# Performance work log

Hardware: AMD Instinct MI355X
Metric: run time of the kernel (lower is better)

Reference implementation:

```python
import jax, jax.numpy as jnp
import numpy as np
from jax import lax

NL = 2        # num mamba layers
D_MODEL = 200
D_STATE = 16
D_CONV = 4
DI = 400      # expand * d_model
DT_RANK = 13  # ceil(d_model / 16)
B = 256
L = 256
EPS = 1e-12


def _ln(x, w, b):
    mu = jnp.mean(x, axis=-1, keepdims=True)
    var = jnp.mean((x - mu) ** 2, axis=-1, keepdims=True)
    return (x - mu) / jnp.sqrt(var + EPS) * w + b


def _mamba(x, in_proj_w, conv_w, conv_b, x_proj_w, dt_proj_w, dt_proj_b, A_log, D, out_proj_w):
    b, l, _ = x.shape
    xz = jnp.einsum('bld,ed->ble', x, in_proj_w)  # [b,l,2*DI]
    xc, z = jnp.split(xz, 2, axis=-1)
    # causal depthwise conv over time (pad d_conv-1 on the left == pytorch pad+slice)
    xt = xc.transpose(0, 2, 1)  # [b,DI,l]
    xt = lax.conv_general_dilated(xt, conv_w[:, None, :], (1,), [(D_CONV - 1, 0)],
                                  dimension_numbers=('NCH', 'OIH', 'NCH'),
                                  feature_group_count=DI)
    xc = jax.nn.silu(xt + conv_b[None, :, None]).transpose(0, 2, 1)  # [b,l,DI]
    x_dbl = jnp.einsum('bld,ed->ble', xc, x_proj_w)  # [b,l,DT_RANK+2*N]
    dt = x_dbl[..., :DT_RANK]
    Bm = x_dbl[..., DT_RANK:DT_RANK + D_STATE]
    Cm = x_dbl[..., DT_RANK + D_STATE:]
    delta = jax.nn.softplus(jnp.einsum('blr,dr->bld', dt, dt_proj_w) + dt_proj_b)  # [b,l,DI]
    A = -jnp.exp(A_log)  # [DI,N]

    def step(h, inp):
        d_t, u_t, B_t, C_t = inp  # [b,DI],[b,DI],[b,N],[b,N]
        dA = jnp.exp(d_t[..., None] * A)  # [b,DI,N]
        h = dA * h + (d_t * u_t)[..., None] * B_t[:, None, :]
        y = jnp.einsum('bdn,bn->bd', h, C_t)
        return h, y

    h0 = jnp.zeros((b, DI, D_STATE), dtype=x.dtype)
    xs = (delta.transpose(1, 0, 2), xc.transpose(1, 0, 2),
          Bm.transpose(1, 0, 2), Cm.transpose(1, 0, 2))
    _, ys = lax.scan(step, h0, xs)
    y = ys.transpose(1, 0, 2) + xc * D  # [b,l,DI]
    y = y * jax.nn.silu(z)
    return jnp.einsum('bld,ed->ble', y, out_proj_w)


def _forward(item_emb, in_proj_w, conv_w, conv_b, x_proj_w, dt_proj_w, dt_proj_b,
             A_log, D, out_proj_w, ln1_w, ln1_b, ffn_w1, ffn_b1, ffn_w2, ffn_b2,
             ffn_ln_w, ffn_ln_b):
    h = item_emb
    for i in range(NL):
        m = _mamba(h, in_proj_w[i], conv_w[i], conv_b[i], x_proj_w[i],
                   dt_proj_w[i], dt_proj_b[i], A_log[i], D[i], out_proj_w[i])
        h = _ln(m + h, ln1_w[i], ln1_b[i])  # num_layers > 1 -> residual branch
        f = jnp.einsum('bld,ed->ble', h, ffn_w1[i]) + ffn_b1[i]
        f = jax.nn.gelu(f, approximate=False)  # torch nn.GELU default = exact
        f = jnp.einsum('ble,de->bld', f, ffn_w2[i]) + ffn_b2[i]
        h = _ln(f + h, ffn_ln_w[i], ffn_ln_b[i])
    c = h[:, -1:, :]
    x_n = h[:, :-1, :]
    return c, x_n


def setup_inputs() -> dict:
    key = jax.random.key(0)
    ks = jax.random.split(key, 10)
    s = 0.02
    f32 = jnp.float32
    A_log = jnp.broadcast_to(jnp.log(jnp.arange(1, D_STATE + 1, dtype=f32)),
                             (NL, DI, D_STATE))
    return {
        'item_emb': jax.random.normal(ks[0], (B, L, D_MODEL), f32),
        'item_seq_len': jax.random.randint(ks[1], (B,), 1, L, jnp.int32),
        'in_proj_w': s * jax.random.normal(ks[2], (NL, 2 * DI, D_MODEL), f32),
        'conv_w': s * jax.random.normal(ks[3], (NL, DI, D_CONV), f32),
        'conv_b': jnp.zeros((NL, DI), f32),
        'x_proj_w': s * jax.random.normal(ks[4], (NL, DT_RANK + 2 * D_STATE, DI), f32),
        'dt_proj_w': s * jax.random.normal(ks[5], (NL, DI, DT_RANK), f32),
        'dt_proj_b': s * jax.random.normal(ks[6], (NL, DI), f32),
        'A_log': A_log,
        'D': jnp.ones((NL, DI), f32),
        'out_proj_w': s * jax.random.normal(ks[7], (NL, D_MODEL, DI), f32),
        'ln1_w': jnp.ones((NL, D_MODEL), f32),
        'ln1_b': jnp.zeros((NL, D_MODEL), f32),
        'ffn_w1': s * jax.random.normal(ks[8], (NL, 4 * D_MODEL, D_MODEL), f32),
        'ffn_b1': jnp.zeros((NL, 4 * D_MODEL), f32),
        'ffn_w2': s * jax.random.normal(ks[9], (NL, D_MODEL, 4 * D_MODEL), f32),
        'ffn_b2': jnp.zeros((NL, D_MODEL), f32),
        'ffn_ln_w': jnp.ones((NL, D_MODEL), f32),
        'ffn_ln_b': jnp.zeros((NL, D_MODEL), f32),
    }


def reference(item_emb, item_seq_len, in_proj_w, conv_w, conv_b, x_proj_w,
              dt_proj_w, dt_proj_b, A_log, D, out_proj_w, ln1_w, ln1_b,
              ffn_w1, ffn_b1, ffn_w2, ffn_b2, ffn_ln_w, ffn_ln_b):
    # item_seq_len is accepted but unused by Mamba4Rec.forward
    return _forward(item_emb, in_proj_w, conv_w, conv_b, x_proj_w, dt_proj_w,
                    dt_proj_b, A_log, D, out_proj_w, ln1_w, ln1_b, ffn_w1,
                    ffn_b1, ffn_w2, ffn_b2, ffn_ln_w, ffn_ln_b)
```

## Files before the change

kernel.cpp:

```cpp
#include <hip/hip_runtime.h>
#include <hip/hip_bf16.h>

#define DM 200
#define DIE 400
#define LSEQ 256
#define NB 256

typedef __hip_bfloat16 bf16;
typedef const float* fp;
typedef __attribute__((ext_vector_type(8))) short short8;
typedef __attribute__((ext_vector_type(4))) short short4_t;
typedef __attribute__((ext_vector_type(4))) float f32x4;

__device__ __forceinline__ float b2f(bf16 x) { return __bfloat162float(x); }
__device__ __forceinline__ bf16  f2b(float x) { return __float2bfloat16(x); }

__device__ __forceinline__ unsigned short f2bbits(float f) {
    union { float f; unsigned int u; } c; c.f = f;
    unsigned int u = c.u;
    unsigned int r = (u + 0x7fffu + ((u >> 16) & 1u)) >> 16;
    return (unsigned short)r;
}
__device__ __forceinline__ void stf(float* p, float v) { *p = v; }
__device__ __forceinline__ void stf(bf16* p, float v) { *p = f2b(v); }

#define W_XP_OFF 320000
#define W_OP_OFF 356000
#define W_F1_OFF 516000
#define W_F2_OFF 836000
#define W_TOTAL  1156000
#define W_BYTES  2312000

__global__ __launch_bounds__(256) void wcvt_kernel(fp a0, fp a1, fp a2, fp a3, fp a4,
                                                   bf16* __restrict__ dst) {
    int g = blockIdx.x * 256 + threadIdx.x;
    if (g >= W_TOTAL / 4) return;
    int idx = g * 4;
    const float* src;
    int off;
    if (idx < W_XP_OFF)      { src = a0; off = idx; }
    else if (idx < W_OP_OFF) { src = a1; off = idx - W_XP_OFF; }
    else if (idx < W_F1_OFF) { src = a2; off = idx - W_OP_OFF; }
    else if (idx < W_F2_OFF) { src = a3; off = idx - W_F1_OFF; }
    else                     { src = a4; off = idx - W_F2_OFF; }
    float4 v = *(const float4*)(src + off);
    short4_t o;
    o.x = (short)f2bbits(v.x); o.y = (short)f2bbits(v.y);
    o.z = (short)f2bbits(v.z); o.w = (short)f2bbits(v.w);
    *(short4_t*)((short*)dst + idx) = o;
}

__global__ __launch_bounds__(256) void cvt_kernel(const float* __restrict__ src,
                                                  bf16* __restrict__ dst, int n4) {
    int g = blockIdx.x * 256 + threadIdx.x;
    if (g >= n4) return;
    int idx = g * 4;
    float4 v = *(const float4*)(src + idx);
    short4_t o;
    o.x = (short)f2bbits(v.x); o.y = (short)f2bbits(v.y);
    o.z = (short)f2bbits(v.z); o.w = (short)f2bbits(v.w);
    *(short4_t*)((short*)dst + idx) = o;
}

template <typename TC, int EPI>
__global__ __launch_bounds__(256) void gemm_mfma(const bf16* __restrict__ A, int lda,
                                                 const bf16* __restrict__ W,
                                                 const float* __restrict__ bias,
                                                 TC* __restrict__ C, int ldc,
                                                 int N, int K) {
    constexpr int LS = 40;
    __shared__ short As[128 * LS];
    __shared__ short Bs[128 * LS];
    const int m0 = blockIdx.x * 128;
    const int n0 = blockIdx.y * 128;
    const int tid = threadIdx.x;
    const int wave = tid >> 6;
    const int lane = tid & 63;
    const int wm = (wave & 1) * 64;
    const int wn = (wave >> 1) * 64;
    const int fm = lane & 15;
    const int quad = lane >> 4;

    f32x4 acc[4][4] = {};

    const int sr = tid >> 1;
    const int sc = (tid & 1) * 16;

    for (int k0 = 0; k0 < K; k0 += 32) {
        {
            const short* src = (const short*)A + (size_t)(m0 + sr) * lda + k0 + sc;
            short* dst = As + sr * LS + sc;
            if (k0 + sc + 16 <= K) {
                *(short8*)dst = *(const short8*)src;
                *(short8*)(dst + 8) = *(const short8*)(src + 8);
            } else {
#pragma unroll
                for (int j = 0; j < 16; ++j)
                    dst[j] = (k0 + sc + j < K) ? src[j] : (short)0;
            }
        }
        {
            short* dst = Bs + sr * LS + sc;
            if (n0 + sr < N) {
                const short* src = (const short*)W + (size_t)(n0 + sr) * K + k0 + sc;
                if (k0 + sc + 16 <= K) {
                    *(short8*)dst = *(const short8*)src;
                    *(short8*)(dst + 8) = *(const short8*)(src + 8);
                } else {
#pragma unroll
                    for (int j = 0; j < 16; ++j)
                        dst[j] = (k0 + sc + j < K) ? src[j] : (short)0;
                }
            } else {
#pragma unroll
                for (int j = 0; j < 16; ++j) dst[j] = 0;
            }
        }
        __syncthreads();
        short8 af[4], bfr[4];
#pragma unroll
        for (int i = 0; i < 4; ++i)
            af[i] = *(const short8*)(As + (wm + i * 16 + fm) * LS + quad * 8);
#pragma unroll
        for (int j = 0; j < 4; ++j)
            bfr[j] = *(const short8*)(Bs + (wn + j * 16 + fm) * LS + quad * 8);
#pragma unroll
        for (int i = 0; i < 4; ++i)
#pragma unroll
            for (int j = 0; j < 4; ++j)
                acc[i][j] = __builtin_amdgcn_mfma_f32_16x16x32_bf16(af[i], bfr[j], acc[i][j], 0, 0, 0);
        __syncthreads();
    }

#pragma unroll
    for (int j = 0; j < 4; ++j) {
        int n = n0 + wn + j * 16 + fm;
        if (n >= N) continue;
        float bv = (EPI == 2 || EPI == 3) ? bias[n] : 0.f;
#pragma unroll
        for (int i = 0; i < 4; ++i) {
#pragma unroll
            for (int r = 0; r < 4; ++r) {
                int m = m0 + wm + i * 16 + quad * 4 + r;
                float v = acc[i][j][r];
                if (EPI == 2) {
                    v += bv;
                    v = 0.5f * v * (1.f + erff(v * 0.70710678118654752f));
                } else if (EPI == 3) {
                    v += bv;
                } else if (EPI == 5) {
                    if (n >= 400) v = v * __builtin_amdgcn_rcpf(1.f + __expf(-v));
                }
                stf(&C[(size_t)m * ldc + n], v);
            }
        }
    }
}

__global__ __launch_bounds__(256) void conv_silu_inplace(bf16* __restrict__ xz,
                                                         const float* __restrict__ cw,
                                                         const float* __restrict__ cb,
                                                         int total ) {
    int idx = blockIdx.x * 256 + threadIdx.x;
    if (idx >= total) return;
    int d = idx % DIE;
    int b = idx / DIE;
    float w0 = cw[d * 4 + 0];
    float w1 = cw[d * 4 + 1];
    float w2 = cw[d * 4 + 2];
    float w3 = cw[d * 4 + 3];
    float bias = cb[d];
    float x0 = 0.f, x1 = 0.f, x2 = 0.f;
    bf16* p = xz + (size_t)b * LSEQ * 800 + d;
    for (int t = 0; t < LSEQ; ++t) {
        float x = b2f(*p);
        float s = bias + w0 * x0 + w1 * x1 + w2 * x2 + w3 * x;
        x0 = x1; x1 = x2; x2 = x;
        float sig = __builtin_amdgcn_rcpf(1.f + __expf(-s));
        *p = f2b(s * sig);
        p += 800;
    }
}

template <bool FAST>
__device__ __forceinline__ void scan_body(const float* __restrict__ rp,
                                          bf16* __restrict__ xp,
                                          const float* Wr, const float* A2,
                                          float bdt, float Dv) {
    float h[16];
#pragma unroll
    for (int n = 0; n < 16; ++n) h[n] = 0.f;

    auto precomp = [&](int o45, int ox,
                       float* Bb, float* Cb, float* dA, float& du, float& ut, float& zs) {
        float dtv = bdt;
#pragma unroll
        for (int r = 0; r < 13; ++r) dtv += Wr[r] * rp[o45 + r];
#pragma unroll
        for (int j = 0; j < 16; ++j) { Bb[j] = rp[o45 + 13 + j]; Cb[j] = rp[o45 + 29 + j]; }
        ut = b2f(xp[ox]);
        zs = b2f(xp[ox + 400]);
        float sp = (dtv > 20.f) ? dtv : __logf(1.f + __expf(dtv));
        if (FAST) {
            float r1 = __expf(-sp);
            float r2 = r1 * r1, r3 = r2 * r1, r4 = r2 * r2;
            float r5 = r4 * r1, r6 = r4 * r2, r7 = r4 * r3, r8 = r4 * r4;
            dA[0] = r1;  dA[1] = r2;  dA[2] = r3;  dA[3] = r4;
            dA[4] = r5;  dA[5] = r6;  dA[6] = r7;  dA[7] = r8;
            dA[8] = r8 * r1;  dA[9] = r8 * r2;  dA[10] = r8 * r3;  dA[11] = r8 * r4;
            dA[12] = r8 * r5; dA[13] = r8 * r6; dA[14] = r8 * r7;  dA[15] = r8 * r8;
        } else {
#pragma unroll
            for (int n = 0; n < 16; ++n) dA[n] = __expf(sp * A2[n]);
        }
        du = sp * ut;
    };
    auto compute = [&](const float* Bb, const float* Cb, const float* dA,
                       float du, float ut, float zs, int ox) {
#pragma unroll
        for (int n = 0; n < 16; ++n) h[n] = dA[n] * h[n] + du * Bb[n];
        float y0 = 0.f, y1 = 0.f, y2 = 0.f, y3 = 0.f;
#pragma unroll
        for (int n = 0; n < 4; ++n) {
            y0 += h[n] * Cb[n];
            y1 += h[4 + n] * Cb[4 + n];
            y2 += h[8 + n] * Cb[8 + n];
            y3 += h[12 + n] * Cb[12 + n];
        }
        float yv = (y0 + y1) + (y2 + y3) + ut * Dv;
        xp[ox] = f2b(yv * zs);
    };

    float BA[16], CA[16], dAA[16], BB[16], CB[16], dAB[16];
    float duA, utA, zsA, duB, utB, zsB;

    precomp(0, 0, BA, CA, dAA, duA, utA, zsA);

    for (int t = 0; t < LSEQ; t += 2) {
        precomp(45, 800, BB, CB, dAB, duB, utB, zsB);
        compute(BA, CA, dAA, duA, utA, zsA, 0);
        if (t + 2 < LSEQ)
            precomp(90, 1600, BA, CA, dAA, duA, utA, zsA);
        compute(BB, CB, dAB, duB, utB, zsB, 800);
        rp += 90; xp += 1600;
    }
}

__global__ __launch_bounds__(256) void scan_kernel(const float* __restrict__ xdbl,
                                                   bf16* __restrict__ xz,
                                                   const float* __restrict__ dt_w,
                                                   const float* __restrict__ dt_b,
                                                   const float* __restrict__ A_log,
                                                   const float* __restrict__ Dw) {
    const int b = blockIdx.x >> 1;
    const int half = blockIdx.x & 1;
    const int tid = threadIdx.x;
    if (tid >= 200) return;
    const int d = half * 200 + tid;

    float A2[16], Wr[13];
    bool fast = true;
#pragma unroll
    for (int n = 0; n < 16; ++n) {
        A2[n] = -__expf(A_log[d * 16 + n]);
        fast = fast && (fabsf(A2[n] + (float)(n + 1)) < 1e-3f);
    }
#pragma unroll
    for (int r = 0; r < 13; ++r) Wr[r] = dt_w[d * 13 + r];
    const float bdt = dt_b[d];
    const float Dv = Dw[d];

    const float* __restrict__ rp = xdbl + (size_t)b * LSEQ * 45;
    bf16* __restrict__ xp = xz + (size_t)b * LSEQ * 800 + d;

    if (fast) scan_body<true>(rp, xp, Wr, A2, bdt, Dv);
    else      scan_body<false>(rp, xp, Wr, A2, bdt, Dv);
}

__global__ __launch_bounds__(256) void ln_res_kernel(const float* __restrict__ xa,
                                                     const float* xb,
                                                     const float* __restrict__ w,
                                                     const float* __restrict__ bias,
                                                     float* dst,
                                                     bf16* __restrict__ dstb, int rows,
                                                     float* __restrict__ outp, int b0) {
    int wave = threadIdx.x >> 6;
    int lane = threadIdx.x & 63;
    int row = blockIdx.x * 4 + wave;
    if (row >= rows) return;
    const float* pa = xa + (size_t)row * DM;
    const float* pb = xb + (size_t)row * DM;
    float v[4];
    float sum = 0.f, sq = 0.f;
#pragma unroll
    for (int i = 0; i < 4; ++i) {
        int c = lane + i * 64;
        float t = 0.f;
        if (c < DM) t = pa[c] + pb[c];
        v[i] = t;
        sum += t;
        sq += t * t;
    }
#pragma unroll
    for (int off = 32; off > 0; off >>= 1) {
        sum += __shfl_down(sum, off);
        sq += __shfl_down(sq, off);
    }
    sum = __shfl(sum, 0);
    sq = __shfl(sq, 0);
    float mu = sum * (1.f / DM);
    float var = fmaxf(sq * (1.f / DM) - mu * mu, 0.f);
    float rstd = rsqrtf(var + 1e-12f);
    if (outp) {
        int bb = b0 + row / LSEQ;
        int l = row % LSEQ;
        float* po = (l == LSEQ - 1)
                        ? outp + (size_t)bb * DM
                        : outp + (size_t)NB * DM + (size_t)(bb * (LSEQ - 1) + l) * DM;
#pragma unroll
        for (int i = 0; i < 4; ++i) {
            int c = lane + i * 64;
            if (c < DM) po[c] = (v[i] - mu) * rstd * w[c] + bias[c];
        }
    } else {
        float* pd = dst + (size_t)row * DM;
        bf16* pdb = dstb + (size_t)row * DM;
#pragma unroll
        for (int i = 0; i < 4; ++i) {
            int c = lane + i * 64;
            if (c < DM) {
                float o = (v[i] - mu) * rstd * w[c] + bias[c];
                pd[c] = o;
                pdb[c] = f2b(o);
            }
        }
    }
}

extern "C" void kernel_launch(void* const* d_in, const int* in_sizes, int n_in,
                              void* d_out, int out_size, void* d_ws, size_t ws_size,
                              hipStream_t stream) {
    fp emb       = (fp)d_in[0];
    fp in_proj_w = (fp)d_in[2];
    fp conv_w    = (fp)d_in[3];
    fp conv_b    = (fp)d_in[4];
    fp x_proj_w  = (fp)d_in[5];
    fp dt_proj_w = (fp)d_in[6];
    fp dt_proj_b = (fp)d_in[7];
    fp A_log     = (fp)d_in[8];
    fp Dw        = (fp)d_in[9];
    fp out_proj_w= (fp)d_in[10];
    fp ln1_w     = (fp)d_in[11];
    fp ln1_b     = (fp)d_in[12];
    fp ffn_w1    = (fp)d_in[13];
    fp ffn_b1    = (fp)d_in[14];
    fp ffn_w2    = (fp)d_in[15];
    fp ffn_b2    = (fp)d_in[16];
    fp ffn_ln_w  = (fp)d_in[17];
    fp ffn_ln_b  = (fp)d_in[18];

    const int cands[8] = {256, 128, 64, 32, 16, 8, 4, 2};
    int cb = 2;
    for (int ci = 0; ci < 8; ++ci) {
        size_t rcx = (size_t)cands[ci] * LSEQ;
        if (rcx * 3780 + W_BYTES + 1024 <= ws_size) { cb = cands[ci]; break; }
    }
    const size_t rc = (size_t)cb * LSEQ;

    bf16*  wb   = (bf16*)d_ws;
    bf16*  xz   = (bf16*)((char*)d_ws + W_BYTES);
    bf16*  hb   = xz + rc * 800;
    float* xdbl = (float*)(hb + rc * 200);
    float* m    = xdbl + rc * 45;
    float* h    = m + rc * 200;

    wcvt_kernel<<<(W_TOTAL / 4 + 255) / 256, 256, 0, stream>>>(
        in_proj_w, x_proj_w, out_proj_w, ffn_w1, ffn_w2, wb);

    const int rcDM = (int)rc * DM;
    const int gm = (int)rc / 128;

    for (int b0 = 0; b0 < NB; b0 += cb) {
        const float* emb_chunk = emb + (size_t)b0 * LSEQ * DM;

        cvt_kernel<<<(rcDM / 4 + 255) / 256, 256, 0, stream>>>(emb_chunk, hb, rcDM / 4);

        for (int i = 0; i < 2; ++i) {
            const bf16* wb_in = wb + (size_t)i * 160000;
            const bf16* wb_xp = wb + W_XP_OFF + (size_t)i * 18000;
            const bf16* wb_op = wb + W_OP_OFF + (size_t)i * 80000;
            const bf16* wb_f1 = wb + W_F1_OFF + (size_t)i * 160000;
            const bf16* wb_f2 = wb + W_F2_OFF + (size_t)i * 160000;
            fp cw    = conv_w + (size_t)i * 400 * 4;
            fp cbp   = conv_b + (size_t)i * 400;
            fp w_dt  = dt_proj_w + (size_t)i * 400 * 13;
            fp b_dt  = dt_proj_b + (size_t)i * 400;
            fp Ai    = A_log + (size_t)i * 400 * 16;
            fp Di    = Dw + (size_t)i * 400;
            fp l1w   = ln1_w + (size_t)i * 200;
            fp l1b   = ln1_b + (size_t)i * 200;
            fp f1b   = ffn_b1 + (size_t)i * 800;
            fp f2b_  = ffn_b2 + (size_t)i * 200;
            fp flw   = ffn_ln_w + (size_t)i * 200;
            fp flb   = ffn_ln_b + (size_t)i * 200;

            const float* hin = (i == 0) ? emb_chunk : h;
            const bool last = (i == 1);

            gemm_mfma<bf16, 5><<<dim3(gm, 7), 256, 0, stream>>>(
                hb, 200, wb_in, nullptr, xz, 800, 800, 200);
            conv_silu_inplace<<<(cb * DIE + 255) / 256, 256, 0, stream>>>(xz, cw, cbp, cb * DIE);
            gemm_mfma<float, 0><<<dim3(gm, 1), 256, 0, stream>>>(
                xz, 800, wb_xp, nullptr, xdbl, 45, 45, 400);
            scan_kernel<<<cb * 2, 256, 0, stream>>>(xdbl, xz, w_dt, b_dt, Ai, Di);
            gemm_mfma<float, 0><<<dim3(gm, 2), 256, 0, stream>>>(
                xz, 800, wb_op, nullptr, m, 200, 200, 400);
            ln_res_kernel<<<rc / 4, 256, 0, stream>>>(m, hin, l1w, l1b, h, hb, (int)rc,
                                                      nullptr, 0);
            gemm_mfma<bf16, 2><<<dim3(gm, 7), 256, 0, stream>>>(
                hb, 200, wb_f1, f1b, xz, 800, 800, 200);
            gemm_mfma<float, 3><<<dim3(gm, 2), 256, 0, stream>>>(
                xz, 800, wb_f2, f2b_, m, 200, 200, 800);
            ln_res_kernel<<<rc / 4, 256, 0, stream>>>(m, h, flw, flb, h, hb, (int)rc,
                                                      last ? (float*)d_out : nullptr, b0);
        }
    }
}
```

Measured before the change: 1.311 ms.

## Split scan state dimension across two lanes per channel with shuffle reduction

The selective-scan kernel now assigns two threads per channel, each owning 8 of the 16 state elements, and combines the partial outputs with a lane shuffle. Blocks grow from 256 to 512 threads. This doubles thread-level parallelism and halves per-thread register pressure for the sequential recurrence, aiming to shorten the scan's critical path. The cost is that the dt projection, softplus and loads are computed redundantly in both lanes, and there is an extra shuffle per step.

Result: no change. 1.307 ms (-0.3%).

```diff
diff --git a/kernel.cpp b/kernel.cpp
--- a/kernel.cpp
+++ b/kernel.cpp
@@ -186,10 +186,12 @@
 __device__ __forceinline__ void scan_body(const float* __restrict__ rp,
                                           bf16* __restrict__ xp,
                                           const float* Wr, const float* A2,
-                                          float bdt, float Dv) {
-    float h[16];
-#pragma unroll
-    for (int n = 0; n < 16; ++n) h[n] = 0.f;
+                                          float bdt, float Dv, int sub) {
+    float h[8];
+#pragma unroll
+    for (int n = 0; n < 8; ++n) h[n] = 0.f;
+    const int nbase = 13 + sub * 8;
+    const int cbase = 29 + sub * 8;
 
     auto precomp = [&](int o45, int ox,
                        float* Bb, float* Cb, float* dA, float& du, float& ut, float& zs) {
@@ -197,7 +199,7 @@
 #pragma unroll
         for (int r = 0; r < 13; ++r) dtv += Wr[r] * rp[o45 + r];
 #pragma unroll
-        for (int j = 0; j < 16; ++j) { Bb[j] = rp[o45 + 13 + j]; Cb[j] = rp[o45 + 29 + j]; }
+        for (int j = 0; j < 8; ++j) { Bb[j] = rp[o45 + nbase + j]; Cb[j] = rp[o45 + cbase + j]; }
         ut = b2f(xp[ox]);
         zs = b2f(xp[ox + 400]);
         float sp = (dtv > 20.f) ? dtv : __logf(1.f + __expf(dtv));
@@ -205,33 +207,34 @@
             float r1 = __expf(-sp);
             float r2 = r1 * r1, r3 = r2 * r1, r4 = r2 * r2;
             float r5 = r4 * r1, r6 = r4 * r2, r7 = r4 * r3, r8 = r4 * r4;
-            dA[0] = r1;  dA[1] = r2;  dA[2] = r3;  dA[3] = r4;
-            dA[4] = r5;  dA[5] = r6;  dA[6] = r7;  dA[7] = r8;
-            dA[8] = r8 * r1;  dA[9] = r8 * r2;  dA[10] = r8 * r3;  dA[11] = r8 * r4;
-            dA[12] = r8 * r5; dA[13] = r8 * r6; dA[14] = r8 * r7;  dA[15] = r8 * r8;
+            float m8 = sub ? r8 : 1.f;
+            dA[0] = r1 * m8; dA[1] = r2 * m8; dA[2] = r3 * m8; dA[3] = r4 * m8;
+            dA[4] = r5 * m8; dA[5] = r6 * m8; dA[6] = r7 * m8; dA[7] = r8 * m8;
         } else {
 #pragma unroll
-            for (int n = 0; n < 16; ++n) dA[n] = __expf(sp * A2[n]);
+            for (int n = 0; n < 8; ++n) dA[n] = __expf(sp * A2[n]);
         }
         du = sp * ut;
     };
     auto compute = [&](const float* Bb, const float* Cb, const float* dA,
                        float du, float ut, float zs, int ox) {
 #pragma unroll
-        for (int n = 0; n < 16; ++n) h[n] = dA[n] * h[n] + du * Bb[n];
-        float y0 = 0.f, y1 = 0.f, y2 = 0.f, y3 = 0.f;
+        for (int n = 0; n < 8; ++n) h[n] = dA[n] * h[n] + du * Bb[n];
+        float y0 = 0.f, y1 = 0.f;
 #pragma unroll
         for (int n = 0; n < 4; ++n) {
             y0 += h[n] * Cb[n];
             y1 += h[4 + n] * Cb[4 + n];
-            y2 += h[8 + n] * Cb[8 + n];
-            y3 += h[12 + n] * Cb[12 + n];
-        }
-        float yv = (y0 + y1) + (y2 + y3) + ut * Dv;
-        xp[ox] = f2b(yv * zs);
+        }
+        float y = y0 + y1;
+        y += __shfl_xor(y, 1);
+        if (sub == 0) {
+            float yv = y + ut * Dv;
+            xp[ox] = f2b(yv * zs);
+        }
     };
 
-    float BA[16], CA[16], dAA[16], BB[16], CB[16], dAB[16];
+    float BA[8], CA[8], dAA[8], BB[8], CB[8], dAB[8];
     float duA, utA, zsA, duB, utB, zsB;
 
     precomp(0, 0, BA, CA, dAA, duA, utA, zsA);
@@ -246,7 +249,7 @@
     }
 }
 
-__global__ __launch_bounds__(256) void scan_kernel(const float* __restrict__ xdbl,
+__global__ __launch_bounds__(512) void scan_kernel(const float* __restrict__ xdbl,
                                                    bf16* __restrict__ xz,
                                                    const float* __restrict__ dt_w,
                                                    const float* __restrict__ dt_b,
@@ -255,15 +258,16 @@
     const int b = blockIdx.x >> 1;
     const int half = blockIdx.x & 1;
     const int tid = threadIdx.x;
-    if (tid >= 200) return;
-    const int d = half * 200 + tid;
-
-    float A2[16], Wr[13];
+    if (tid >= 400) return;
+    const int d = half * 200 + (tid >> 1);
+    const int sub = tid & 1;
+
+    float A2[8], Wr[13];
     bool fast = true;
 #pragma unroll
-    for (int n = 0; n < 16; ++n) {
-        A2[n] = -__expf(A_log[d * 16 + n]);
-        fast = fast && (fabsf(A2[n] + (float)(n + 1)) < 1e-3f);
+    for (int n = 0; n < 8; ++n) {
+        A2[n] = -__expf(A_log[d * 16 + sub * 8 + n]);
+        fast = fast && (fabsf(A2[n] + (float)(sub * 8 + n + 1)) < 1e-3f);
     }
 #pragma unroll
     for (int r = 0; r < 13; ++r) Wr[r] = dt_w[d * 13 + r];
@@ -273,8 +277,8 @@
     const float* __restrict__ rp = xdbl + (size_t)b * LSEQ * 45;
     bf16* __restrict__ xp = xz + (size_t)b * LSEQ * 800 + d;
 
-    if (fast) scan_body<true>(rp, xp, Wr, A2, bdt, Dv);
-    else      scan_body<false>(rp, xp, Wr, A2, bdt, Dv);
+    if (fast) scan_body<true>(rp, xp, Wr, A2, bdt, Dv, sub);
+    else      scan_body<false>(rp, xp, Wr, A2, bdt, Dv, sub);
 }
 
 __global__ __launch_bounds__(256) void ln_res_kernel(const float* __restrict__ xa,
@@ -412,7 +416,7 @@
             conv_silu_inplace<<<(cb * DIE + 255) / 256, 256, 0, stream>>>(xz, cw, cbp, cb * DIE);
             gemm_mfma<float, 0><<<dim3(gm, 1), 256, 0, stream>>>(
                 xz, 800, wb_xp, nullptr, xdbl, 45, 45, 400);
-            scan_kernel<<<cb * 2, 256, 0, stream>>>(xdbl, xz, w_dt, b_dt, Ai, Di);
+            scan_kernel<<<cb * 2, 512, 0, stream>>>(xdbl, xz, w_dt, b_dt, Ai, Di);
             gemm_mfma<float, 0><<<dim3(gm, 2), 256, 0, stream>>>(
                 xz, 800, wb_op, nullptr, m, 200, 200, 400);
             ln_res_kernel<<<rc / 4, 256, 0, stream>>>(m, hin, l1w, l1b, h, hb, (int)rc,
```

## Fuse residual add and LayerNorm into N=200 projection GEMM epilogue

Applied to the files above, without the earlier changes.

Adds a gemm_ln kernel in which each block computes a full 128x200 output tile (256-wide N tile). Its epilogue adds bias and the residual, reduces row mean and variance through shuffles and shared memory, and writes the normalized fp32, bf16 or final output directly. This replaces the out_proj and ffn_w2 GEMMs plus the separate ln_res kernels, removing the intermediate m buffer round trip and two launches per layer. The cost is fewer blocks (grid gm instead of gm*2), 32 accumulators per thread, and a larger chunk size from the reduced workspace need. In the ffn_w2 case the kernel reads R and writes dst at the same address h, which is safe because each element is read by the same thread before that thread writes it.

Result: slower. 1.454 ms (+10.9%).

```diff
diff --git a/kernel.cpp b/kernel.cpp
--- a/kernel.cpp
+++ b/kernel.cpp
@@ -136,7 +136,7 @@
     for (int j = 0; j < 4; ++j) {
         int n = n0 + wn + j * 16 + fm;
         if (n >= N) continue;
-        float bv = (EPI == 2 || EPI == 3) ? bias[n] : 0.f;
+        float bv = (EPI == 2) ? bias[n] : 0.f;
 #pragma unroll
         for (int i = 0; i < 4; ++i) {
 #pragma unroll
@@ -146,8 +146,6 @@
                 if (EPI == 2) {
                     v += bv;
                     v = 0.5f * v * (1.f + erff(v * 0.70710678118654752f));
-                } else if (EPI == 3) {
-                    v += bv;
                 } else if (EPI == 5) {
                     if (n >= 400) v = v * __builtin_amdgcn_rcpf(1.f + __expf(-v));
                 }
@@ -155,6 +153,156 @@
             }
         }
     }
+}
+
+template <int BIAS>
+__global__ __launch_bounds__(256, 2) void gemm_ln(const bf16* __restrict__ A, int lda,
+                                                  const bf16* __restrict__ W,
+                                                  const float* __restrict__ bias,
+                                                  const float* __restrict__ R,
+                                                  const float* __restrict__ lw,
+                                                  const float* __restrict__ lb,
+                                                  float* dst, bf16* __restrict__ dstb,
+                                                  float* __restrict__ outp, int b0,
+                                                  int K) {
+    constexpr int LS = 40;
+    __shared__ short As[128 * LS];
+    __shared__ short Bs[256 * LS];
+    __shared__ float red[128][2][2];
+    const int m0 = blockIdx.x * 128;
+    const int tid = threadIdx.x;
+    const int wave = tid >> 6;
+    const int lane = tid & 63;
+    const int wm = (wave & 1) * 64;
+    const int wn = (wave >> 1) * 128;
+    const int fm = lane & 15;
+    const int quad = lane >> 4;
+
+    f32x4 acc[4][8] = {};
+
+    const int sr = tid >> 1;
+    const int sc = (tid & 1) * 16;
+
+    if (tid >= 200) {
+        short* z = Bs + tid * LS;
+#pragma unroll
+        for (int j = 0; j < 32; ++j) z[j] = 0;
+    }
+
+    for (int k0 = 0; k0 < K; k0 += 32) {
+        {
+            const short* src = (const short*)A + (size_t)(m0 + sr) * lda + k0 + sc;
+            short* dstA = As + sr * LS + sc;
+            if (k0 + sc + 16 <= K) {
+                *(short8*)dstA = *(const short8*)src;
+                *(short8*)(dstA + 8) = *(const short8*)(src + 8);
+            } else {
+#pragma unroll
+                for (int j = 0; j < 16; ++j)
+                    dstA[j] = (k0 + sc + j < K) ? src[j] : (short)0;
+            }
+        }
+        if (tid < 200) {
+            const short* src = (const short*)W + (size_t)tid * K + k0;
+            short* dstB = Bs + tid * LS;
+            if (k0 + 32 <= K) {
+                *(short8*)dstB = *(const short8*)src;
+                *(short8*)(dstB + 8) = *(const short8*)(src + 8);
+                *(short8*)(dstB + 16) = *(const short8*)(src + 16);
+                *(short8*)(dstB + 24) = *(const short8*)(src + 24);
+            } else {
+#pragma unroll
+                for (int j = 0; j < 32; ++j)
+                    dstB[j] = (k0 + j < K) ? src[j] : (short)0;
+            }
+        }
+        __syncthreads();
+        short8 af[4], bfr[8];
+#pragma unroll
+        for (int i = 0; i < 4; ++i)
+            af[i] = *(const short8*)(As + (wm + i * 16 + fm) * LS + quad * 8);
+#pragma unroll
+        for (int j = 0; j < 8; ++j)
+            bfr[j] = *(const short8*)(Bs + (wn + j * 16 + fm) * LS + quad * 8);
+#pragma unroll
+        for (int i = 0; i < 4; ++i)
+#pragma unroll
+            for (int j = 0; j < 8; ++j)
+                acc[i][j] = __builtin_amdgcn_mfma_f32_16x16x32_bf16(af[i], bfr[j], acc[i][j], 0, 0, 0);
+        __syncthreads();
+    }
+
+#pragma unroll
+    for (int j = 0; j < 8; ++j) {
+        int n = wn + j * 16 + fm;
+        if (n >= DM) continue;
+        float bv = BIAS ? bias[n] : 0.f;
+#pragma unroll
+        for (int i = 0; i < 4; ++i)
+#pragma unroll
+            for (int r = 0; r < 4; ++r) {
+                int m = m0 + wm + i * 16 + quad * 4 + r;
+                acc[i][j][r] += bv + R[(size_t)m * DM + n];
+            }
+    }
+#pragma unroll
+    for (int i = 0; i < 4; ++i)
+#pragma unroll
+        for (int r = 0; r < 4; ++r) {
+            float s = 0.f, q = 0.f;
+#pragma unroll
+            for (int j = 0; j < 8; ++j) {
+                int n = wn + j * 16 + fm;
+                if (n < DM) { float v = acc[i][j][r]; s += v; q += v * v; }
+            }
+#pragma unroll
+            for (int off = 8; off >= 1; off >>= 1) {
+                s += __shfl_xor(s, off);
+                q += __shfl_xor(q, off);
+            }
+            if (fm == 0) {
+                int row = wm + i * 16 + quad * 4 + r;
+                red[row][wn >> 7][0] = s;
+                red[row][wn >> 7][1] = q;
+            }
+        }
+    __syncthreads();
+#pragma unroll
+    for (int i = 0; i < 4; ++i)
+#pragma unroll
+        for (int r = 0; r < 4; ++r) {
+            int row = wm + i * 16 + quad * 4 + r;
+            float s = red[row][0][0] + red[row][1][0];
+            float q = red[row][0][1] + red[row][1][1];
+            float mu = s * (1.f / DM);
+            float var = fmaxf(q * (1.f / DM) - mu * mu, 0.f);
+            float rstd = rsqrtf(var + 1e-12f);
+            int m = m0 + row;
+            if (outp) {
+                int bb = b0 + m / LSEQ;
+                int l = m % LSEQ;
+                float* po = (l == LSEQ - 1)
+                                ? outp + (size_t)bb * DM
+                                : outp + (size_t)NB * DM + (size_t)(bb * (LSEQ - 1) + l) * DM;
+#pragma unroll
+                for (int j = 0; j < 8; ++j) {
+                    int n = wn + j * 16 + fm;
+                    if (n < DM) po[n] = (acc[i][j][r] - mu) * rstd * lw[n] + lb[n];
+                }
+            } else {
+                float* pd = dst + (size_t)m * DM;
+                bf16* pdb = dstb + (size_t)m * DM;
+#pragma unroll
+                for (int j = 0; j < 8; ++j) {
+                    int n = wn + j * 16 + fm;
+                    if (n < DM) {
+                        float o = (acc[i][j][r] - mu) * rstd * lw[n] + lb[n];
+                        pd[n] = o;
+                        pdb[n] = f2b(o);
+                    }
+                }
+            }
+        }
 }
 
 __global__ __launch_bounds__(256) void conv_silu_inplace(bf16* __restrict__ xz,
@@ -277,66 +425,6 @@
     else      scan_body<false>(rp, xp, Wr, A2, bdt, Dv);
 }
 
-__global__ __launch_bounds__(256) void ln_res_kernel(const float* __restrict__ xa,
-                                                     const float* xb,
-                                                     const float* __restrict__ w,
-                                                     const float* __restrict__ bias,
-                                                     float* dst,
-                                                     bf16* __restrict__ dstb, int rows,
-                                                     float* __restrict__ outp, int b0) {
-    int wave = threadIdx.x >> 6;
-    int lane = threadIdx.x & 63;
-    int row = blockIdx.x * 4 + wave;
-    if (row >= rows) return;
-    const float* pa = xa + (size_t)row * DM;
-    const float* pb = xb + (size_t)row * DM;
-    float v[4];
-    float sum = 0.f, sq = 0.f;
-#pragma unroll
-    for (int i = 0; i < 4; ++i) {
-        int c = lane + i * 64;
-        float t = 0.f;
-        if (c < DM) t = pa[c] + pb[c];
-        v[i] = t;
-        sum += t;
-        sq += t * t;
-    }
-#pragma unroll
-    for (int off = 32; off > 0; off >>= 1) {
-        sum += __shfl_down(sum, off);
-        sq += __shfl_down(sq, off);
-    }
-    sum = __shfl(sum, 0);
-    sq = __shfl(sq, 0);
-    float mu = sum * (1.f / DM);
-    float var = fmaxf(sq * (1.f / DM) - mu * mu, 0.f);
-    float rstd = rsqrtf(var + 1e-12f);
-    if (outp) {
-        int bb = b0 + row / LSEQ;
-        int l = row % LSEQ;
-        float* po = (l == LSEQ - 1)
-                        ? outp + (size_t)bb * DM
-                        : outp + (size_t)NB * DM + (size_t)(bb * (LSEQ - 1) + l) * DM;
-#pragma unroll
-        for (int i = 0; i < 4; ++i) {
-            int c = lane + i * 64;
-            if (c < DM) po[c] = (v[i] - mu) * rstd * w[c] + bias[c];
-        }
-    } else {
-        float* pd = dst + (size_t)row * DM;
-        bf16* pdb = dstb + (size_t)row * DM;
-#pragma unroll
-        for (int i = 0; i < 4; ++i) {
-            int c = lane + i * 64;
-            if (c < DM) {
-                float o = (v[i] - mu) * rstd * w[c] + bias[c];
-                pd[c] = o;
-                pdb[c] = f2b(o);
-            }
-        }
-    }
-}
-
 extern "C" void kernel_launch(void* const* d_in, const int* in_sizes, int n_in,
                               void* d_out, int out_size, void* d_ws, size_t ws_size,
                               hipStream_t stream) {
@@ -363,7 +451,7 @@
     int cb = 2;
     for (int ci = 0; ci < 8; ++ci) {
         size_t rcx = (size_t)cands[ci] * LSEQ;
-        if (rcx * 3780 + W_BYTES + 1024 <= ws_size) { cb = cands[ci]; break; }
+        if (rcx * 2980 + W_BYTES + 4096 <= ws_size) { cb = cands[ci]; break; }
     }
     const size_t rc = (size_t)cb * LSEQ;
 
@@ -371,8 +459,7 @@
     bf16*  xz   = (bf16*)((char*)d_ws + W_BYTES);
     bf16*  hb   = xz + rc * 800;
     float* xdbl = (float*)(hb + rc * 200);
-    float* m    = xdbl + rc * 45;
-    float* h    = m + rc * 200;
+    float* h    = xdbl + rc * 45;
 
     wcvt_kernel<<<(W_TOTAL / 4 + 255) / 256, 256, 0, stream>>>(
         in_proj_w, x_proj_w, out_proj_w, ffn_w1, ffn_w2, wb);
@@ -413,16 +500,13 @@
             gemm_mfma<float, 0><<<dim3(gm, 1), 256, 0, stream>>>(
                 xz, 800, wb_xp, nullptr, xdbl, 45, 45, 400);
             scan_kernel<<<cb * 2, 256, 0, stream>>>(xdbl, xz, w_dt, b_dt, Ai, Di);
-            gemm_mfma<float, 0><<<dim3(gm, 2), 256, 0, stream>>>(
-                xz, 800, wb_op, nullptr, m, 200, 200, 400);
-            ln_res_kernel<<<rc / 4, 256, 0, stream>>>(m, hin, l1w, l1b, h, hb, (int)rc,
-                                                      nullptr, 0);
+            gemm_ln<0><<<gm, 256, 0, stream>>>(
+                xz, 800, wb_op, nullptr, hin, l1w, l1b, h, hb, nullptr, 0, 400);
             gemm_mfma<bf16, 2><<<dim3(gm, 7), 256, 0, stream>>>(
                 hb, 200, wb_f1, f1b, xz, 800, 800, 200);
-            gemm_mfma<float, 3><<<dim3(gm, 2), 256, 0, stream>>>(
-                xz, 800, wb_f2, f2b_, m, 200, 200, 800);
-            ln_res_kernel<<<rc / 4, 256, 0, stream>>>(m, h, flw, flb, h, hb, (int)rc,
-                                                      last ? (float*)d_out : nullptr, b0);
-        }
-    }
-}
+            gemm_ln<1><<<gm, 256, 0, stream>>>(
+                xz, 800, wb_f2, f2b_, h, flw, flb, h, hb,
+                last ? (float*)d_out : nullptr, b0, 800);
+        }
+    }
+}
```
